# Kernel optimization log

Measured on AMD Instinct MI355X. Metric: run time of the kernel, lower is better.

The kernel has to match this reference:

```python
import jax, jax.numpy as jnp
import numpy as np

DIM = 2048
NUM_HEADS = 16
HEAD_DIM = DIM // NUM_HEADS  # 128
LC = HEAD_DIM // 2           # 64 complex pairs per head
B, S = 2, 2048
EPS = 1e-6


def setup_inputs() -> dict:
    key = jax.random.key(0)
    ks = jax.random.split(key, 12)
    x = jax.random.normal(ks[0], (B, S, DIM), dtype=jnp.float32)
    # freqs: unit-modulus complex rotations stored as (cos, sin), shape [S,1,LC,2]
    theta = jax.random.uniform(ks[1], (S, 1, LC), dtype=jnp.float32) * (2.0 * np.pi)
    freqs = jnp.stack([jnp.cos(theta), jnp.sin(theta)], axis=-1)
    scale = 0.02
    wq = jax.random.normal(ks[2], (DIM, DIM), dtype=jnp.float32) * scale
    bq = jnp.zeros((DIM,), dtype=jnp.float32)
    wk = jax.random.normal(ks[3], (DIM, DIM), dtype=jnp.float32) * scale
    bk = jnp.zeros((DIM,), dtype=jnp.float32)
    wv = jax.random.normal(ks[4], (DIM, DIM), dtype=jnp.float32) * scale
    bv = jnp.zeros((DIM,), dtype=jnp.float32)
    wo = jax.random.normal(ks[5], (DIM, DIM), dtype=jnp.float32) * scale
    bo = jnp.zeros((DIM,), dtype=jnp.float32)
    gq = jnp.ones((DIM,), dtype=jnp.float32)   # RMSNorm weight for q
    gk = jnp.ones((DIM,), dtype=jnp.float32)   # RMSNorm weight for k
    return {"x": x, "freqs": freqs, "wq": wq, "bq": bq, "wk": wk, "bk": bk,
            "wv": wv, "bv": bv, "wo": wo, "bo": bo, "gq": gq, "gk": gk}


def _rms_norm(x, g):
    xf = x.astype(jnp.float32)
    y = xf * jax.lax.rsqrt(jnp.mean(xf * xf, axis=-1, keepdims=True) + EPS)
    return y.astype(x.dtype) * g


def _rope_apply(x, freqs):
    # x: [B,S,D] -> complex pairs [B,S,H,LC,2]; freqs: [S,1,LC,2] (cos,sin)
    b, s, _ = x.shape
    xp = x.astype(jnp.float32).reshape(b, s, NUM_HEADS, LC, 2)
    xr, xi = xp[..., 0], xp[..., 1]
    cr = freqs[None, :, :, :, 0]  # [1,S,1,LC]
    ci = freqs[None, :, :, :, 1]
    out_r = xr * cr - xi * ci
    out_i = xr * ci + xi * cr
    out = jnp.stack([out_r, out_i], axis=-1).reshape(b, s, DIM)
    return out.astype(x.dtype)


def _attention(q, k, v):
    # q,k,v: [B,S,D] -> multihead SDPA -> [B,S,D]
    b, s, _ = q.shape
    qh = q.reshape(b, s, NUM_HEADS, HEAD_DIM).transpose(0, 2, 1, 3)
    kh = k.reshape(b, s, NUM_HEADS, HEAD_DIM).transpose(0, 2, 1, 3)
    vh = v.reshape(b, s, NUM_HEADS, HEAD_DIM).transpose(0, 2, 1, 3)
    scale = 1.0 / np.sqrt(HEAD_DIM).astype(np.float32)
    scores = jnp.einsum('bhqd,bhkd->bhqk', qh, kh) * scale
    probs = jax.nn.softmax(scores, axis=-1)
    out = jnp.einsum('bhqk,bhkd->bhqd', probs, vh)
    return out.transpose(0, 2, 1, 3).reshape(b, s, DIM)


def reference(x, freqs, wq, bq, wk, bk, wv, bv, wo, bo, gq, gk):
    q = _rms_norm(x @ wq.T + bq, gq)
    k = _rms_norm(x @ wk.T + bk, gk)
    v = x @ wv.T + bv
    q = _rope_apply(q, freqs)
    k = _rope_apply(k, freqs)
    attn = _attention(q, k, v)
    return attn @ wo.T + bo
```

## Files before the change

### kernel.cpp

```cpp
#include <hip/hip_runtime.h>
#include <cstdint>

typedef __bf16 bf16;
typedef __bf16 bf16x8 __attribute__((ext_vector_type(8)));
typedef __bf16 bf16x4 __attribute__((ext_vector_type(4)));
typedef float f32x4 __attribute__((ext_vector_type(4)));

#define DIMN 2048
#define SEQ  2048
#define NH   16
#define HD   128

__device__ __forceinline__ void gld_lds16(const bf16* g, bf16* l) {
    __builtin_amdgcn_global_load_lds(
        (const __attribute__((address_space(1))) void*)g,
        (__attribute__((address_space(3))) void*)l,
        16, 0, 0);
}

__global__ __launch_bounds__(256) void cast_f32_bf16(const float* __restrict__ src,
                                                     bf16* __restrict__ dst, int n4) {
    int i = blockIdx.x * 256 + threadIdx.x;
    if (i < n4) {
        float4 v = ((const float4*)src)[i];
        bf16x4 o;
        o[0] = (bf16)v.x; o[1] = (bf16)v.y; o[2] = (bf16)v.z; o[3] = (bf16)v.w;
        ((bf16x4*)dst)[i] = o;
    }
}

template<int OUT_F32>
__global__ __launch_bounds__(256) void gemm_bt(
    const bf16* __restrict__ A,
    const bf16* __restrict__ Bw0, const bf16* __restrict__ Bw1, const bf16* __restrict__ Bw2,
    const float* __restrict__ bias0, const float* __restrict__ bias1, const float* __restrict__ bias2,
    void* __restrict__ C0, void* __restrict__ C1, void* __restrict__ C2)
{
    const int K = DIMN, N = DIMN;
    const bf16* Bw = Bw0; const float* bias = bias0; void* Cout = C0;
    if (blockIdx.z == 1) { Bw = Bw1; bias = bias1; Cout = C1; }
    if (blockIdx.z == 2) { Bw = Bw2; bias = bias2; Cout = C2; }

    __shared__ __attribute__((aligned(16))) bf16 As[128 * 32];
    __shared__ __attribute__((aligned(16))) bf16 Bs[128 * 32];

    const int t    = threadIdx.x;
    const int lane = t & 63, wave = t >> 6;
    const int l15  = lane & 15, quad = lane >> 4;
    const int wm   = (wave >> 1) * 64, wn = (wave & 1) * 64;
    const long bm  = (long)blockIdx.y * 128;
    const long bn  = (long)blockIdx.x * 128;

    const int  srow = t >> 2;
    const int  scol = (t & 3) * 8;
    const bf16* ag0 = A  + (bm + srow) * (long)K + scol;
    const bf16* ag1 = A  + (bm + 64 + srow) * (long)K + scol;
    const bf16* bg0 = Bw + (bn + srow) * (long)K + scol;
    const bf16* bg1 = Bw + (bn + 64 + srow) * (long)K + scol;
    bf16* asd = As + t * 8;
    bf16* bsd = Bs + t * 8;

    f32x4 acc[4][4] = {};

    for (int k0 = 0; k0 < K; k0 += 32) {
        gld_lds16(ag0 + k0, asd);
        gld_lds16(ag1 + k0, asd + 2048);
        gld_lds16(bg0 + k0, bsd);
        gld_lds16(bg1 + k0, bsd + 2048);
        __syncthreads();

        bf16x8 af[4], bfr[4];
#pragma unroll
        for (int i = 0; i < 4; i++)
            af[i] = *(const bf16x8*)(As + (wm + i * 16 + l15) * 32 + quad * 8);
#pragma unroll
        for (int j = 0; j < 4; j++)
            bfr[j] = *(const bf16x8*)(Bs + (wn + j * 16 + l15) * 32 + quad * 8);
#pragma unroll
        for (int i = 0; i < 4; i++)
#pragma unroll
            for (int j = 0; j < 4; j++)
                acc[i][j] = __builtin_amdgcn_mfma_f32_16x16x32_bf16(af[i], bfr[j], acc[i][j], 0, 0, 0);
        __syncthreads();
    }

#pragma unroll
    for (int j = 0; j < 4; j++) {
        const long col = bn + wn + j * 16 + l15;
        const float bv = bias[col];
#pragma unroll
        for (int i = 0; i < 4; i++) {
            const long row0 = bm + wm + i * 16 + quad * 4;
#pragma unroll
            for (int r = 0; r < 4; r++) {
                float v = acc[i][j][r] + bv;
                if (OUT_F32) ((float*)Cout)[(row0 + r) * N + col] = v;
                else         ((bf16*)Cout)[(row0 + r) * N + col] = (bf16)v;
            }
        }
    }
}

__global__ __launch_bounds__(256) void rmsnorm_rope(
    bf16* __restrict__ q, bf16* __restrict__ k,
    const float* __restrict__ gq, const float* __restrict__ gk,
    const float* __restrict__ freqs)
{
    const int row = blockIdx.x;
    bf16* ptr = blockIdx.y ? k : q;
    const float* g = blockIdx.y ? gk : gq;
    const int s = row & (SEQ - 1);
    const int t = threadIdx.x;
    const int lane = t & 63, wave = t >> 6;

    bf16* base = ptr + (long)row * DIMN + t * 8;
    bf16x8 raw = *(const bf16x8*)base;
    float v[8]; float ss = 0.f;
#pragma unroll
    for (int j = 0; j < 8; j++) { v[j] = (float)raw[j]; ss += v[j] * v[j]; }
#pragma unroll
    for (int off = 32; off; off >>= 1) ss += __shfl_xor(ss, off, 64);
    __shared__ float red[4];
    if (lane == 0) red[wave] = ss;
    __syncthreads();
    float tot = red[0] + red[1] + red[2] + red[3];
    float rn = rsqrtf(tot * (1.0f / DIMN) + 1e-6f);

    const int e0 = t * 8;
    bf16x8 o;
#pragma unroll
    for (int pp = 0; pp < 4; pp++) {
        int e = e0 + pp * 2;
        float xr = v[pp * 2]     * rn * g[e];
        float xi = v[pp * 2 + 1] * rn * g[e + 1];
        int lc = (e >> 1) & 63;
        float cr = freqs[s * 128 + lc * 2];
        float ci = freqs[s * 128 + lc * 2 + 1];
        o[pp * 2]     = (bf16)(xr * cr - xi * ci);
        o[pp * 2 + 1] = (bf16)(xr * ci + xi * cr);
    }
    *(bf16x8*)base = o;
}

__global__ __launch_bounds__(256) void transpose_v(const bf16* __restrict__ vin,
                                                   bf16* __restrict__ vt)
{
    __shared__ float tile[64][65];
    const int b = blockIdx.z, st = blockIdx.x, ct = blockIdx.y;
    const int tx = threadIdx.x & 63, ty = threadIdx.x >> 6;
#pragma unroll
    for (int ii = 0; ii < 16; ii++) {
        int r = ii * 4 + ty;
        tile[r][tx] = (float)vin[((long)(b * SEQ + st * 64 + r)) * DIMN + ct * 64 + tx];
    }
    __syncthreads();
#pragma unroll
    for (int ii = 0; ii < 16; ii++) {
        int c = ii * 4 + ty;
        vt[((long)(b * DIMN + ct * 64 + c)) * SEQ + st * 64 + tx] = (bf16)tile[tx][c];
    }
}

__global__ __launch_bounds__(256, 2) void attention(
    const bf16* __restrict__ Q, const bf16* __restrict__ Kb,
    const bf16* __restrict__ Vt, bf16* __restrict__ O)
{
    __shared__ __attribute__((aligned(16))) bf16 Ksh[64 * 136];
    __shared__ __attribute__((aligned(16))) bf16 Vsh[128 * 72];
    __shared__ __attribute__((aligned(16))) bf16 Psh[4][32 * 72];

    const int t = threadIdx.x;
    const int lane = t & 63, wave = t >> 6;
    const int l15 = lane & 15, quad = lane >> 4;
    const int bh = blockIdx.y, b = bh >> 4, h = bh & 15;
    const int qt = blockIdx.x;
    const long qrow0 = (long)b * SEQ + qt * 128 + wave * 32;
    const bf16* qbase = Q  + qrow0 * DIMN + h * HD;
    const bf16* kbase = Kb + (long)b * SEQ * DIMN + h * HD;
    const bf16* vbase = Vt + (long)bh * HD * SEQ;

    bf16x8 qf[2][4];
#pragma unroll
    for (int i = 0; i < 2; i++)
#pragma unroll
        for (int kd = 0; kd < 4; kd++)
            qf[i][kd] = *(const bf16x8*)(qbase + (long)(i * 16 + l15) * DIMN + kd * 32 + quad * 8);

    f32x4 o_acc[2][8] = {};
    float L[2][4] = {};
    const float scale = 0.08838834764831845f;

    for (int kt = 0; kt < 32; kt++) {
#pragma unroll
        for (int it = 0; it < 4; it++) {
            int fs = it * 256 + t;
            int kr = fs >> 4, ks = fs & 15;
            *(uint4*)(Ksh + kr * 136 + ks * 8) =
                *(const uint4*)(kbase + (long)(kt * 64 + kr) * DIMN + ks * 8);
            int dr = fs >> 3, vs = fs & 7;
            *(uint4*)(Vsh + dr * 72 + vs * 8) =
                *(const uint4*)(vbase + (long)dr * SEQ + kt * 64 + vs * 8);
        }
        __syncthreads();

        f32x4 sc[2][4] = {};
#pragma unroll
        for (int j = 0; j < 4; j++)
#pragma unroll
            for (int kd = 0; kd < 4; kd++) {
                bf16x8 bfr = *(const bf16x8*)(Ksh + (j * 16 + l15) * 136 + kd * 32 + quad * 8);
                sc[0][j] = __builtin_amdgcn_mfma_f32_16x16x32_bf16(qf[0][kd], bfr, sc[0][j], 0, 0, 0);
                sc[1][j] = __builtin_amdgcn_mfma_f32_16x16x32_bf16(qf[1][kd], bfr, sc[1][j], 0, 0, 0);
            }

#pragma unroll
        for (int i = 0; i < 2; i++) {
            float rsum[4] = {0.f, 0.f, 0.f, 0.f};
#pragma unroll
            for (int j = 0; j < 4; j++)
#pragma unroll
                for (int r = 0; r < 4; r++) {
                    float e = __expf(sc[i][j][r] * scale);
                    rsum[r] += e;
                    Psh[wave][(i * 16 + quad * 4 + r) * 72 + j * 16 + l15] = (bf16)e;
                }
#pragma unroll
            for (int r = 0; r < 4; r++) {
                float vv = rsum[r];
                vv += __shfl_xor(vv, 1, 64);
                vv += __shfl_xor(vv, 2, 64);
                vv += __shfl_xor(vv, 4, 64);
                vv += __shfl_xor(vv, 8, 64);
                L[i][r] += vv;
            }
        }
        __syncthreads();

#pragma unroll
        for (int kd = 0; kd < 2; kd++) {
            bf16x8 pa[2];
            pa[0] = *(const bf16x8*)(Psh[wave] + (l15)      * 72 + kd * 32 + quad * 8);
            pa[1] = *(const bf16x8*)(Psh[wave] + (16 + l15) * 72 + kd * 32 + quad * 8);
#pragma unroll
            for (int dj = 0; dj < 8; dj++) {
                bf16x8 vfr = *(const bf16x8*)(Vsh + (dj * 16 + l15) * 72 + kd * 32 + quad * 8);
                o_acc[0][dj] = __builtin_amdgcn_mfma_f32_16x16x32_bf16(pa[0], vfr, o_acc[0][dj], 0, 0, 0);
                o_acc[1][dj] = __builtin_amdgcn_mfma_f32_16x16x32_bf16(pa[1], vfr, o_acc[1][dj], 0, 0, 0);
            }
        }
        __syncthreads();
    }

#pragma unroll
    for (int i = 0; i < 2; i++)
#pragma unroll
        for (int r = 0; r < 4; r++) {
            float inv = 1.0f / L[i][r];
            long orow = qrow0 + i * 16 + quad * 4 + r;
#pragma unroll
            for (int dj = 0; dj < 8; dj++)
                O[orow * DIMN + h * HD + dj * 16 + l15] = (bf16)(o_acc[i][dj][r] * inv);
        }
}

extern "C" void kernel_launch(void* const* d_in, const int* in_sizes, int n_in,
                              void* d_out, int out_size, void* d_ws, size_t ws_size,
                              hipStream_t stream) {
    const float* x     = (const float*)d_in[0];
    const float* freqs = (const float*)d_in[1];
    const float* wq    = (const float*)d_in[2];
    const float* bq    = (const float*)d_in[3];
    const float* wk    = (const float*)d_in[4];
    const float* bk    = (const float*)d_in[5];
    const float* wv    = (const float*)d_in[6];
    const float* bv    = (const float*)d_in[7];
    const float* wo    = (const float*)d_in[8];
    const float* bo    = (const float*)d_in[9];
    const float* gq    = (const float*)d_in[10];
    const float* gk    = (const float*)d_in[11];
    float* out = (float*)d_out;

    const size_t MAT  = (size_t)4096 * 2048 * 2;
    const size_t WMAT = (size_t)2048 * 2048 * 2;
    char* p = (char*)d_ws;
    bf16* xb  = (bf16*)p; p += MAT;
    bf16* wqb = (bf16*)p; p += WMAT;
    bf16* wkb = (bf16*)p; p += WMAT;
    bf16* wvb = (bf16*)p; p += WMAT;
    bf16* wob = (bf16*)p; p += WMAT;
    bf16* qb  = (bf16*)p; p += MAT;
    bf16* kb  = (bf16*)p; p += MAT;
    bf16* vb  = (bf16*)p; p += MAT;
    bf16* vt  = (bf16*)p; p += MAT;
    bf16* attn = qb;

    cast_f32_bf16<<<8192, 256, 0, stream>>>(x,  xb,  2097152);
    cast_f32_bf16<<<4096, 256, 0, stream>>>(wq, wqb, 1048576);
    cast_f32_bf16<<<4096, 256, 0, stream>>>(wk, wkb, 1048576);
    cast_f32_bf16<<<4096, 256, 0, stream>>>(wv, wvb, 1048576);
    cast_f32_bf16<<<4096, 256, 0, stream>>>(wo, wob, 1048576);

    gemm_bt<0><<<dim3(16, 32, 3), 256, 0, stream>>>(xb, wqb, wkb, wvb,
                                                    bq, bk, bv, qb, kb, vb);
    rmsnorm_rope<<<dim3(4096, 2), 256, 0, stream>>>(qb, kb, gq, gk, freqs);
    transpose_v<<<dim3(32, 32, 2), 256, 0, stream>>>(vb, vt);
    attention<<<dim3(16, 32), 256, 0, stream>>>(qb, kb, vt, attn);
    gemm_bt<1><<<dim3(16, 32, 1), 256, 0, stream>>>(attn, wob, wob, wob,
                                                    bo, bo, bo, out, out, out);
}
```

Baseline: 483.3 us.

## Swizzle GEMM and attention LDS layouts, merge weight casts, drop barrier

Applies XOR swizzles to the GEMM A/B shared tiles and to the per-wave P buffer in attention, so that the MFMA fragment reads avoid LDS bank conflicts. Because each wave writes and reads only its own P buffer, the barrier between the softmax and the PV product is removed. The four weight-cast launches are merged into one 2D launch to cut launch overhead. The swizzle must match on the global_load_lds write side and on the read side. Dropping the barrier depends on the wave-local P buffer being safe with no block sync.

```diff
diff --git a/kernel.cpp b/kernel.cpp
--- a/kernel.cpp
+++ b/kernel.cpp
@@ -20,6 +20,24 @@
 
 __global__ __launch_bounds__(256) void cast_f32_bf16(const float* __restrict__ src,
                                                      bf16* __restrict__ dst, int n4) {
+    int i = blockIdx.x * 256 + threadIdx.x;
+    if (i < n4) {
+        float4 v = ((const float4*)src)[i];
+        bf16x4 o;
+        o[0] = (bf16)v.x; o[1] = (bf16)v.y; o[2] = (bf16)v.z; o[3] = (bf16)v.w;
+        ((bf16x4*)dst)[i] = o;
+    }
+}
+
+__global__ __launch_bounds__(256) void cast_w4(
+    const float* __restrict__ s0, const float* __restrict__ s1,
+    const float* __restrict__ s2, const float* __restrict__ s3,
+    bf16* __restrict__ d0, bf16* __restrict__ d1,
+    bf16* __restrict__ d2, bf16* __restrict__ d3, int n4) {
+    const float* src = s0; bf16* dst = d0;
+    if (blockIdx.y == 1) { src = s1; dst = d1; }
+    if (blockIdx.y == 2) { src = s2; dst = d2; }
+    if (blockIdx.y == 3) { src = s3; dst = d3; }
     int i = blockIdx.x * 256 + threadIdx.x;
     if (i < n4) {
         float4 v = ((const float4*)src)[i];
@@ -52,7 +70,8 @@
     const long bn  = (long)blockIdx.x * 128;
 
     const int  srow = t >> 2;
-    const int  scol = (t & 3) * 8;
+    const int  sseg = (t & 3) ^ ((srow >> 1) & 3);
+    const int  scol = sseg * 8;
     const bf16* ag0 = A  + (bm + srow) * (long)K + scol;
     const bf16* ag1 = A  + (bm + 64 + srow) * (long)K + scol;
     const bf16* bg0 = Bw + (bn + srow) * (long)K + scol;
@@ -60,6 +79,8 @@
     bf16* asd = As + t * 8;
     bf16* bsd = Bs + t * 8;
 
+    const int sw = (quad ^ ((l15 >> 1) & 3)) * 8;
+
     f32x4 acc[4][4] = {};
 
     for (int k0 = 0; k0 < K; k0 += 32) {
@@ -72,10 +93,10 @@
         bf16x8 af[4], bfr[4];
 #pragma unroll
         for (int i = 0; i < 4; i++)
-            af[i] = *(const bf16x8*)(As + (wm + i * 16 + l15) * 32 + quad * 8);
+            af[i] = *(const bf16x8*)(As + (wm + i * 16 + l15) * 32 + sw);
 #pragma unroll
         for (int j = 0; j < 4; j++)
-            bfr[j] = *(const bf16x8*)(Bs + (wn + j * 16 + l15) * 32 + quad * 8);
+            bfr[j] = *(const bf16x8*)(Bs + (wn + j * 16 + l15) * 32 + sw);
 #pragma unroll
         for (int i = 0; i < 4; i++)
 #pragma unroll
@@ -189,6 +210,7 @@
     f32x4 o_acc[2][8] = {};
     float L[2][4] = {};
     const float scale = 0.08838834764831845f;
+    const int rkey = (l15 >> 2) & 3;
 
     for (int kt = 0; kt < 32; kt++) {
 #pragma unroll
@@ -217,13 +239,16 @@
         for (int i = 0; i < 2; i++) {
             float rsum[4] = {0.f, 0.f, 0.f, 0.f};
 #pragma unroll
-            for (int j = 0; j < 4; j++)
+            for (int j = 0; j < 4; j++) {
+                const int seg = 2 * j + (l15 >> 3);
+                const int segS = seg ^ quad;
 #pragma unroll
                 for (int r = 0; r < 4; r++) {
                     float e = __expf(sc[i][j][r] * scale);
                     rsum[r] += e;
-                    Psh[wave][(i * 16 + quad * 4 + r) * 72 + j * 16 + l15] = (bf16)e;
+                    Psh[wave][(i * 16 + quad * 4 + r) * 72 + segS * 8 + (l15 & 7)] = (bf16)e;
                 }
+            }
 #pragma unroll
             for (int r = 0; r < 4; r++) {
                 float vv = rsum[r];
@@ -234,13 +259,12 @@
                 L[i][r] += vv;
             }
         }
-        __syncthreads();
 
 #pragma unroll
         for (int kd = 0; kd < 2; kd++) {
             bf16x8 pa[2];
-            pa[0] = *(const bf16x8*)(Psh[wave] + (l15)      * 72 + kd * 32 + quad * 8);
-            pa[1] = *(const bf16x8*)(Psh[wave] + (16 + l15) * 72 + kd * 32 + quad * 8);
+            pa[0] = *(const bf16x8*)(Psh[wave] + (l15)      * 72 + ((kd * 4 + quad) ^ rkey) * 8);
+            pa[1] = *(const bf16x8*)(Psh[wave] + (16 + l15) * 72 + ((kd * 4 + quad) ^ rkey) * 8);
 #pragma unroll
             for (int dj = 0; dj < 8; dj++) {
                 bf16x8 vfr = *(const bf16x8*)(Vsh + (dj * 16 + l15) * 72 + kd * 32 + quad * 8);
@@ -294,11 +318,8 @@
     bf16* vt  = (bf16*)p; p += MAT;
     bf16* attn = qb;
 
-    cast_f32_bf16<<<8192, 256, 0, stream>>>(x,  xb,  2097152);
-    cast_f32_bf16<<<4096, 256, 0, stream>>>(wq, wqb, 1048576);
-    cast_f32_bf16<<<4096, 256, 0, stream>>>(wk, wkb, 1048576);
-    cast_f32_bf16<<<4096, 256, 0, stream>>>(wv, wvb, 1048576);
-    cast_f32_bf16<<<4096, 256, 0, stream>>>(wo, wob, 1048576);
+    cast_f32_bf16<<<8192, 256, 0, stream>>>(x, xb, 2097152);
+    cast_w4<<<dim3(4096, 4), 256, 0, stream>>>(wq, wk, wv, wo, wqb, wkb, wvb, wob, 1048576);
 
     gemm_bt<0><<<dim3(16, 32, 3), 256, 0, stream>>>(xb, wqb, wkb, wvb,
                                                     bq, bk, bv, qb, kb, vb);
```

Result: faster. 469.3 us (-2.9%).
